# Kernel tuning notes

Measured on AMD Instinct MI355X. Metric: run time of the kernel, lower is better.

Reference implementation:

```python
import jax, jax.numpy as jnp
import numpy as np

B, T, D, H, STRIDE, MLP = 2, 2048, 1024, 16, 8, 4096
HD = D // H
EPS = 1e-5


def _ln(x, g, b):
    m = x.mean(-1, keepdims=True)
    v = x.var(-1, keepdims=True)
    return (x - m) * jax.lax.rsqrt(v + EPS) * g + b


def setup_inputs() -> dict:
    key = jax.random.key(0)
    ks = jax.random.split(key, 6)
    s = lambda k, shape: (jax.random.normal(k, shape, jnp.float32) * 0.02)
    return {
        "x": jax.random.normal(ks[0], (B, T, D), jnp.float32),
        "w_in": s(ks[1], (3 * D, D)),   # torch in_proj_weight
        "b_in": jnp.zeros((3 * D,), jnp.float32),
        "w_out": s(ks[2], (D, D)),      # attn out_proj
        "b_out": jnp.zeros((D,), jnp.float32),
        "w1": s(ks[3], (MLP, D)),       # mlp first Linear (torch layout [out,in])
        "b1": jnp.zeros((MLP,), jnp.float32),
        "w2": s(ks[4], (D, MLP)),       # mlp second Linear
        "b2": jnp.zeros((D,), jnp.float32),
        "ln1_g": jnp.ones((D,), jnp.float32),
        "ln1_b": jnp.zeros((D,), jnp.float32),
        "ln2_g": jnp.ones((D,), jnp.float32),
        "ln2_b": jnp.zeros((D,), jnp.float32),
    }


def reference(x, w_in, b_in, w_out, b_out, w1, b1, w2, b2,
              ln1_g, ln1_b, ln2_g, ln2_b):
    Bs, Ts, Ds = x.shape
    xn = _ln(x, ln1_g, ln1_b)
    # fused qkv projection (torch Linear: y = x @ W.T + b)
    qkv = xn @ w_in.T + b_in                              # [B,T,3D]
    q, k, v = jnp.split(qkv, 3, axis=-1)
    to_heads = lambda t: t.reshape(Bs, Ts, H, HD).transpose(0, 2, 1, 3)
    q, k, v = to_heads(q), to_heads(k), to_heads(v)       # [B,H,T,hd]
    scores = jnp.einsum("bhqd,bhkd->bhqk", q, k) / jnp.sqrt(jnp.float32(HD))
    # mask: rows at multiples of STRIDE attend everywhere; others only to self
    idx = jnp.arange(Ts)
    allowed = ((idx % STRIDE) == 0)[:, None] | (idx[:, None] == idx[None, :])
    scores = jnp.where(allowed, scores, -jnp.inf)
    attn = jax.nn.softmax(scores, axis=-1)
    o = jnp.einsum("bhqk,bhkd->bhqd", attn, v)            # [B,H,T,hd]
    o = o.transpose(0, 2, 1, 3).reshape(Bs, Ts, Ds)
    o = o @ w_out.T + b_out
    x = x + o
    xn = _ln(x, ln2_g, ln2_b)
    h = jax.nn.gelu(xn @ w1.T + b1, approximate=False)    # torch nn.GELU default = exact
    x = x + (h @ w2.T + b2)
    return x
```

## Files before the change

kernel.cpp:

```cpp
#include <hip/hip_runtime.h>

#define D_ 1024
#define T_ 2048
#define B_ 2
#define H_ 16
#define MLP_ 4096
#define NTOK (B_*T_)
#define QG 256
#define L2E 1.44269504088896340736f

typedef float f32x4 __attribute__((ext_vector_type(4)));
typedef __bf16 bf16x8 __attribute__((ext_vector_type(8)));

__device__ __forceinline__ unsigned short f2bf(float f) {
  unsigned int u = __float_as_uint(f);
  u += 0x7fff + ((u >> 16) & 1);
  return (unsigned short)(u >> 16);
}

__device__ __forceinline__ float wave_sum(float v) {
  for (int o = 32; o > 0; o >>= 1) v += __shfl_down(v, o, 64);
  return v;
}

__device__ __forceinline__ void gload16(const unsigned short* g, unsigned short* l) {
  __builtin_amdgcn_global_load_lds(
      (const __attribute__((address_space(1))) void*)g,
      (__attribute__((address_space(3))) void*)l, 16, 0, 0);
}

#define N4_WIN  786432
#define N4_WOUT 262144
#define N4_W1   1048576
#define N4_W2   1048576
__global__ void cast_all_kernel(const float* __restrict__ w_in,
                                const float* __restrict__ w_out,
                                const float* __restrict__ w1,
                                const float* __restrict__ w2,
                                unsigned short* __restrict__ o_in,
                                unsigned short* __restrict__ o_out,
                                unsigned short* __restrict__ o1,
                                unsigned short* __restrict__ o2) {
  int i = blockIdx.x * 256 + threadIdx.x;
  const float* src; unsigned short* dst; int j = i;
  if (i < N4_WIN) { src = w_in; dst = o_in; }
  else if ((j -= N4_WIN) < N4_WOUT) { src = w_out; dst = o_out; }
  else if ((j -= N4_WOUT) < N4_W1) { src = w1; dst = o1; }
  else { j -= N4_W1; src = w2; dst = o2; }
  float4 v = ((const float4*)src)[j];
  ushort4 o;
  o.x = f2bf(v.x); o.y = f2bf(v.y); o.z = f2bf(v.z); o.w = f2bf(v.w);
  ((ushort4*)dst)[j] = o;
}

__global__ void ln_kernel(const float* __restrict__ x, const float* __restrict__ g,
                          const float* __restrict__ b, unsigned short* __restrict__ out) {
  int row = blockIdx.x;
  int tid = threadIdx.x;
  int wave = tid >> 6, lane = tid & 63;
  float4 v = ((const float4*)(x + (size_t)row * D_))[tid];
  float s  = v.x + v.y + v.z + v.w;
  float s2 = v.x*v.x + v.y*v.y + v.z*v.z + v.w*v.w;
  s = wave_sum(s); s2 = wave_sum(s2);
  __shared__ float r1[4], r2[4];
  if (lane == 0) { r1[wave] = s; r2[wave] = s2; }
  __syncthreads();
  float ts  = r1[0] + r1[1] + r1[2] + r1[3];
  float ts2 = r2[0] + r2[1] + r2[2] + r2[3];
  float mean = ts * (1.0f / D_);
  float var  = ts2 * (1.0f / D_) - mean * mean;
  float rs = rsqrtf(var + 1e-5f);
  float4 gv = ((const float4*)g)[tid];
  float4 bv = ((const float4*)b)[tid];
  ushort4 o;
  o.x = f2bf((v.x - mean) * rs * gv.x + bv.x);
  o.y = f2bf((v.y - mean) * rs * gv.y + bv.y);
  o.z = f2bf((v.z - mean) * rs * gv.z + bv.z);
  o.w = f2bf((v.w - mean) * rs * gv.w + bv.w);
  ((ushort4*)(out + (size_t)row * D_))[tid] = o;
}

__global__ void reduce_ln_kernel(const float* __restrict__ part,
                                 const float* __restrict__ x,
                                 const float* __restrict__ bias,
                                 const float* __restrict__ g,
                                 const float* __restrict__ b,
                                 float* __restrict__ x1,
                                 unsigned short* __restrict__ xn2) {
  int row = blockIdx.x;
  int tid = threadIdx.x;
  int wave = tid >> 6, lane = tid & 63;
  size_t base = (size_t)row * (D_ / 4) + tid;
  float4 v = ((const float4*)x)[base];
  float4 bo = ((const float4*)bias)[tid];
  v.x += bo.x; v.y += bo.y; v.z += bo.z; v.w += bo.w;
#pragma unroll
  for (int c = 0; c < 2; ++c) {
    float4 p = ((const float4*)part)[(size_t)c * (NTOK * (D_ / 4)) + base];
    v.x += p.x; v.y += p.y; v.z += p.z; v.w += p.w;
  }
  ((float4*)x1)[base] = v;
  float s  = v.x + v.y + v.z + v.w;
  float s2 = v.x*v.x + v.y*v.y + v.z*v.z + v.w*v.w;
  s = wave_sum(s); s2 = wave_sum(s2);
  __shared__ float r1[4], r2[4];
  if (lane == 0) { r1[wave] = s; r2[wave] = s2; }
  __syncthreads();
  float ts  = r1[0] + r1[1] + r1[2] + r1[3];
  float ts2 = r2[0] + r2[1] + r2[2] + r2[3];
  float mean = ts * (1.0f / D_);
  float var  = ts2 * (1.0f / D_) - mean * mean;
  float rs = rsqrtf(var + 1e-5f);
  float4 gv = ((const float4*)g)[tid];
  float4 bv = ((const float4*)b)[tid];
  ushort4 o;
  o.x = f2bf((v.x - mean) * rs * gv.x + bv.x);
  o.y = f2bf((v.y - mean) * rs * gv.y + bv.y);
  o.z = f2bf((v.z - mean) * rs * gv.z + bv.z);
  o.w = f2bf((v.w - mean) * rs * gv.w + bv.w);
  ((ushort4*)xn2)[base] = o;
}

__global__ void reduce_out_kernel(const float* __restrict__ part,
                                  const float* __restrict__ x1,
                                  const float* __restrict__ bias,
                                  float* __restrict__ out) {
  int i = blockIdx.x * 256 + threadIdx.x;
  float4 v = ((const float4*)x1)[i];
  float4 bo = ((const float4*)bias)[i & (D_ / 4 - 1)];
  v.x += bo.x; v.y += bo.y; v.z += bo.z; v.w += bo.w;
#pragma unroll
  for (int c = 0; c < 4; ++c) {
    float4 p = ((const float4*)part)[(size_t)c * (NTOK * (D_ / 4)) + i];
    v.x += p.x; v.y += p.y; v.z += p.z; v.w += p.w;
  }
  ((float4*)out)[i] = v;
}

template<int EPI, int SWIZ, int LDA, int LDB, int LDC>
__global__ __launch_bounds__(256)
void gemm_kernel(const unsigned short* __restrict__ A, size_t sA,
                 const unsigned short* __restrict__ Bm, size_t sB,
                 void* __restrict__ Cv, size_t sC,
                 const float* __restrict__ bias,
                 unsigned short* __restrict__ aux1,
                 unsigned short* __restrict__ aux2,
                 int K, int nx, int ny, int kshift) {
  __shared__ __align__(16) unsigned short As[128 * 64];
  __shared__ __align__(16) unsigned short Bs[128 * 64];
  const int flat = blockIdx.x;
  int bx, by;
  if (SWIZ == 1) {
    bx = flat / ny; by = flat - bx * ny;
  } else {
    const int sxc = nx >> 1;
    const int nSuper = sxc * (ny >> 2);
    int s = flat % nSuper, pos = flat / nSuper;
    int sx = s % sxc, sy = s / sxc;
    bx = sx * 2 + (pos & 1);
    by = sy * 4 + (pos >> 1);
  }
  const int bz = blockIdx.z;
  const int batch = bz >> kshift;
  const int kOff  = (bz & ((1 << kshift) - 1)) * K;
  const int m0 = by * 128;
  const int n0 = bx * 128;
  const int tid = threadIdx.x;
  const int lane = tid & 63, wave = tid >> 6;
  const int wm = (wave >> 1) * 64, wn = (wave & 1) * 64;
  const int fr = lane & 15, q = lane >> 4;
  const int f0 = ((q)     ^ (fr & 7)) << 3;
  const int f1 = ((4 + q) ^ (fr & 7)) << 3;

  const unsigned short* aP[4];
  const unsigned short* bP[4];
  unsigned short* dA[4];
  unsigned short* dB[4];
#pragma unroll
  for (int p = 0; p < 4; ++p) {
    int l = p * 256 + tid;
    int r = l >> 3;
    int cg = (l & 7) ^ (r & 7);
    aP[p] = A  + (size_t)batch * sA + kOff + (size_t)(m0 + r) * LDA + cg * 8;
    bP[p] = Bm + (size_t)batch * sB + kOff + (size_t)(n0 + r) * LDB + cg * 8;
    dA[p] = &As[l * 8];
    dB[p] = &Bs[l * 8];
  }

  f32x4 acc[4][4] = {};
  for (int ko = 0; ko < K; ko += 64) {
    __syncthreads();
#pragma unroll
    for (int p = 0; p < 4; ++p) {
      gload16(aP[p], dA[p]); gload16(bP[p], dB[p]);
      aP[p] += 64; bP[p] += 64;
    }
    __syncthreads();
    {
      bf16x8 af[4], bfr[4];
#pragma unroll
      for (int i = 0; i < 4; ++i) af[i]  = *(const bf16x8*)&As[(wm + i * 16 + fr) * 64 + f0];
#pragma unroll
      for (int j = 0; j < 4; ++j) bfr[j] = *(const bf16x8*)&Bs[(wn + j * 16 + fr) * 64 + f0];
#pragma unroll
      for (int i = 0; i < 4; ++i)
#pragma unroll
        for (int j = 0; j < 4; ++j)
          acc[i][j] = __builtin_amdgcn_mfma_f32_16x16x32_bf16(af[i], bfr[j], acc[i][j], 0, 0, 0);
    }
    {
      bf16x8 af[4], bfr[4];
#pragma unroll
      for (int i = 0; i < 4; ++i) af[i]  = *(const bf16x8*)&As[(wm + i * 16 + fr) * 64 + f1];
#pragma unroll
      for (int j = 0; j < 4; ++j) bfr[j] = *(const bf16x8*)&Bs[(wn + j * 16 + fr) * 64 + f1];
#pragma unroll
      for (int i = 0; i < 4; ++i)
#pragma unroll
        for (int j = 0; j < 4; ++j)
          acc[i][j] = __builtin_amdgcn_mfma_f32_16x16x32_bf16(af[i], bfr[j], acc[i][j], 0, 0, 0);
    }
  }

  const int col = lane & 15, rbase = (lane >> 4) * 4;
#pragma unroll
  for (int i = 0; i < 4; ++i) {
#pragma unroll
    for (int j = 0; j < 4; ++j) {
      int gn = n0 + wn + j * 16 + col;
      int gmb = m0 + wm + i * 16 + rbase;
      float bv = (EPI == 2 || EPI == 8) ? bias[gn] : 0.0f;
#pragma unroll
      for (int r = 0; r < 4; ++r) {
        int gm = gmb + r;
        float v = acc[i][j][r] + bv;
        if (EPI == 2) {
          float u = v * (1.5957691216f + 0.0713548162f * v * v);
          float gl = v / (1.0f + exp2f(-L2E * u));
          ((unsigned short*)Cv)[(size_t)gm * LDC + gn] = f2bf(gl);
        } else if (EPI == 7) {
          ((float*)Cv)[(size_t)bz * sC + (size_t)gm * LDC + gn] = v;
        } else if (EPI == 8) {
          int sec = gn >> 10;
          int hh = (gn >> 6) & (H_ - 1);
          int dd = gn & 63;
          int t = gm & (T_ - 1);
          int b = gm >> 11;
          unsigned short bf = f2bf(v);
          if (sec == 0) {
            if (!(t & 7))
              aux1[(((size_t)(b * H_ + hh)) * QG + (t >> 3)) * 64 + dd] = bf;
          } else if (sec == 1) {
            aux2[(((size_t)(b * H_ + hh)) * T_ + t) * 64 + dd] = bf;
          } else {
            ((unsigned short*)Cv)[(size_t)gm * D_ + (gn - 2 * D_)] = bf;
          }
        }
      }
    }
  }
}

template<int EPI>
__global__ __launch_bounds__(512)
void gemm256_kernel(const unsigned short* __restrict__ A, int LDA,
                    const unsigned short* __restrict__ Bm, int LDB,
                    void* __restrict__ Cv, size_t sC, int LDC,
                    const float* __restrict__ bias, int K, int nxs) {
  __shared__ __align__(16) unsigned short As[2 * 16384];
  __shared__ __align__(16) unsigned short Bs[2 * 16384];
  const int tid = threadIdx.x;
  const int lane = tid & 63, w = tid >> 6;
  const int wm = w >> 2, wn = w & 3;
  const int fr = lane & 15, q = lane >> 4, xr = fr & 7;

  const int nwg = gridDim.x;
  const int bid = blockIdx.x;
  const int l = (bid & 7) * (nwg >> 3) + (bid >> 3);
  const int bx = l & ((1 << nxs) - 1), by = l >> nxs;
  const int m0 = by * 256, n0 = bx * 256;
  const int kOff = blockIdx.z * K;

  const unsigned short* aS[4];
  const unsigned short* bS[4];
#pragma unroll
  for (int s = 0; s < 4; ++s) {
    int ls = s * 512 + tid;
    int r = ls >> 3;
    int cg = (ls & 7) ^ (r & 7);
    aS[s] = A  + (size_t)(m0 + r) * LDA + kOff + cg * 8;
    bS[s] = Bm + (size_t)(n0 + r) * LDB + kOff + cg * 8;
  }
  const int NT = K >> 6;

#pragma unroll
  for (int s = 0; s < 4; ++s) {
    gload16(aS[s], &As[s * 4096 + tid * 8]);
    gload16(bS[s], &Bs[s * 4096 + tid * 8]);
  }
#pragma unroll
  for (int s = 0; s < 4; ++s) {
    gload16(aS[s] + 64, &As[16384 + s * 4096 + tid * 8]);
    gload16(bS[s] + 64, &Bs[16384 + s * 4096 + tid * 8]);
  }
  asm volatile("s_waitcnt vmcnt(8)");
  __builtin_amdgcn_sched_barrier(0);
  __builtin_amdgcn_s_barrier();
  __builtin_amdgcn_sched_barrier(0);

  const int aOff = ((wm * 128 + fr) << 7) + ((q ^ xr) << 4);
  const int bOff = ((wn * 64 + fr) << 7) + ((q ^ xr) << 4);

  f32x4 acc[8][4] = {};

  for (int t = 0; t < NT; ++t) {
    const int cb = (t & 1) << 15;
    const char* Ab = (const char*)As + cb;
    const char* Bb = (const char*)Bs + cb;
    unsigned short* Ad = (unsigned short*)((char*)As + cb);
    unsigned short* Bd = (unsigned short*)((char*)Bs + cb);
    const int ko2 = (t + 2) << 6;
    bf16x8 af[2][4], bfr[2][4];

#pragma unroll
    for (int i = 0; i < 4; ++i) {
      af[0][i] = *(const bf16x8*)(Ab + aOff + i * 2048);
      af[1][i] = *(const bf16x8*)(Ab + (aOff ^ 64) + i * 2048);
    }
#pragma unroll
    for (int j = 0; j < 2; ++j) {
      bfr[0][j] = *(const bf16x8*)(Bb + bOff + j * 2048);
      bfr[1][j] = *(const bf16x8*)(Bb + (bOff ^ 64) + j * 2048);
    }
    __builtin_amdgcn_sched_barrier(0);
    __builtin_amdgcn_s_barrier();
    __builtin_amdgcn_sched_barrier(0);
    __builtin_amdgcn_s_setprio(1);
#pragma unroll
    for (int i = 0; i < 4; ++i)
#pragma unroll
      for (int j = 0; j < 2; ++j) {
        acc[i][j] = __builtin_amdgcn_mfma_f32_16x16x32_bf16(af[0][i], bfr[0][j], acc[i][j], 0, 0, 0);
        acc[i][j] = __builtin_amdgcn_mfma_f32_16x16x32_bf16(af[1][i], bfr[1][j], acc[i][j], 0, 0, 0);
      }
    __builtin_amdgcn_s_setprio(0);
    __builtin_amdgcn_sched_barrier(0);
    __builtin_amdgcn_s_barrier();
    __builtin_amdgcn_sched_barrier(0);

#pragma unroll
    for (int j = 2; j < 4; ++j) {
      bfr[0][j] = *(const bf16x8*)(Bb + bOff + j * 2048);
      bfr[1][j] = *(const bf16x8*)(Bb + (bOff ^ 64) + j * 2048);
    }
    if (t + 2 < NT) {
      gload16(aS[0] + ko2, Ad + tid * 8);
      gload16(aS[2] + ko2, Ad + 2 * 4096 + tid * 8);
    }
    __builtin_amdgcn_sched_barrier(0);
    __builtin_amdgcn_s_barrier();
    __builtin_amdgcn_sched_barrier(0);
    __builtin_amdgcn_s_setprio(1);
#pragma unroll
    for (int i = 0; i < 4; ++i)
#pragma unroll
      for (int j = 0; j < 2; ++j) {
        acc[i][2 + j] = __builtin_amdgcn_mfma_f32_16x16x32_bf16(af[0][i], bfr[0][2 + j], acc[i][2 + j], 0, 0, 0);
        acc[i][2 + j] = __builtin_amdgcn_mfma_f32_16x16x32_bf16(af[1][i], bfr[1][2 + j], acc[i][2 + j], 0, 0, 0);
      }
    __builtin_amdgcn_s_setprio(0);
    __builtin_amdgcn_sched_barrier(0);
    __builtin_amdgcn_s_barrier();
    __builtin_amdgcn_sched_barrier(0);

#pragma unroll
    for (int i = 0; i < 4; ++i) {
      af[0][i] = *(const bf16x8*)(Ab + (aOff + 8192) + i * 2048);
      af[1][i] = *(const bf16x8*)(Ab + ((aOff + 8192) ^ 64) + i * 2048);
    }
    if (t + 2 < NT) {
      gload16(bS[0] + ko2, Bd + tid * 8);
      gload16(bS[1] + ko2, Bd + 4096 + tid * 8);
      gload16(bS[2] + ko2, Bd + 2 * 4096 + tid * 8);
      gload16(bS[3] + ko2, Bd + 3 * 4096 + tid * 8);
    }
    __builtin_amdgcn_sched_barrier(0);
    __builtin_amdgcn_s_barrier();
    __builtin_amdgcn_sched_barrier(0);
    __builtin_amdgcn_s_setprio(1);
#pragma unroll
    for (int i = 0; i < 4; ++i)
#pragma unroll
      for (int j = 0; j < 2; ++j) {
        acc[4 + i][j] = __builtin_amdgcn_mfma_f32_16x16x32_bf16(af[0][i], bfr[0][j], acc[4 + i][j], 0, 0, 0);
        acc[4 + i][j] = __builtin_amdgcn_mfma_f32_16x16x32_bf16(af[1][i], bfr[1][j], acc[4 + i][j], 0, 0, 0);
      }
    __builtin_amdgcn_s_setprio(0);
    __builtin_amdgcn_sched_barrier(0);
    __builtin_amdgcn_s_barrier();
    __builtin_amdgcn_sched_barrier(0);

    if (t + 2 < NT) {
      gload16(aS[1] + ko2, Ad + 4096 + tid * 8);
      gload16(aS[3] + ko2, Ad + 3 * 4096 + tid * 8);
    }
    if (t + 1 < NT) {
      if (t + 2 < NT) asm volatile("s_waitcnt vmcnt(8)");
      else            asm volatile("s_waitcnt vmcnt(0)");
    }
    __builtin_amdgcn_sched_barrier(0);
    __builtin_amdgcn_s_barrier();
    __builtin_amdgcn_sched_barrier(0);
    __builtin_amdgcn_s_setprio(1);
#pragma unroll
    for (int i = 0; i < 4; ++i)
#pragma unroll
      for (int j = 0; j < 2; ++j) {
        acc[4 + i][2 + j] = __builtin_amdgcn_mfma_f32_16x16x32_bf16(af[0][i], bfr[0][2 + j], acc[4 + i][2 + j], 0, 0, 0);
        acc[4 + i][2 + j] = __builtin_amdgcn_mfma_f32_16x16x32_bf16(af[1][i], bfr[1][2 + j], acc[4 + i][2 + j], 0, 0, 0);
      }
    __builtin_amdgcn_s_setprio(0);
    __builtin_amdgcn_sched_barrier(0);
    __builtin_amdgcn_s_barrier();
    __builtin_amdgcn_sched_barrier(0);
  }

  const int col = lane & 15, rbase = (lane >> 4) * 4;
  const int gm0 = m0 + wm * 128 + rbase;
  const int gn0 = n0 + wn * 64 + col;
#pragma unroll
  for (int mi = 0; mi < 8; ++mi) {
#pragma unroll
    for (int j = 0; j < 4; ++j) {
      int gn = gn0 + j * 16;
      float bv = (EPI == 2) ? bias[gn] : 0.0f;
#pragma unroll
      for (int r = 0; r < 4; ++r) {
        int gm = gm0 + mi * 16 + r;
        float v = acc[mi][j][r] + bv;
        if (EPI == 2) {
          float u = v * (1.5957691216f + 0.0713548162f * v * v);
          float gl = v / (1.0f + exp2f(-L2E * u));
          ((unsigned short*)Cv)[(size_t)gm * LDC + gn] = f2bf(gl);
        } else {
          ((float*)Cv)[(size_t)blockIdx.z * sC + (size_t)gm * LDC + gn] = v;
        }
      }
    }
  }
}

__global__ void vtrans_kernel(const unsigned short* __restrict__ vcomp,
                              unsigned short* __restrict__ Vt) {
  int blk = blockIdx.x;
  int tchunk = blk & 31;
  int bh = blk >> 5;
  int h = bh & (H_ - 1), b = bh >> 4;
  int t0 = tchunk * 64;
  __shared__ unsigned short ls[64][66];
  int tid = threadIdx.x;
#pragma unroll
  for (int it = 0; it < 16; ++it) {
    int linear = it * 256 + tid;
    int d = linear & 63, tl = linear >> 6;
    ls[d][tl] = vcomp[((size_t)(b * T_ + t0 + tl)) * D_ + h * 64 + d];
  }
  __syncthreads();
#pragma unroll
  for (int it = 0; it < 16; ++it) {
    int linear = it * 256 + tid;
    int tl = linear & 63, d = linear >> 6;
    Vt[((size_t)(bh * 64 + d)) * T_ + t0 + tl] = ls[d][tl];
  }
}

__global__ __launch_bounds__(256)
void flash_kernel(const unsigned short* __restrict__ Qg,
                  const unsigned short* __restrict__ Kh,
                  const unsigned short* __restrict__ Vt,
                  float* __restrict__ Opart,
                  float* __restrict__ ml) {
  const int kc = blockIdx.x, qt = blockIdx.y, bh = blockIdx.z;
  const int tid = threadIdx.x;
  const int lane = tid & 63, w = tid >> 6;
  const int fr = lane & 15, quad = lane >> 4;

  __shared__ __align__(16) unsigned short Qs[64 * 64];
  __shared__ __align__(16) unsigned short Ks[128 * 64];
  __shared__ __align__(16) unsigned short Vs[64 * 128];
  __shared__ __align__(16) unsigned short Ps[4 * 16 * 128];

  const unsigned short* Qbase = Qg + ((size_t)bh * 256 + qt * 64) * 64;
#pragma unroll
  for (int p = 0; p < 2; ++p) {
    int linear = p * 256 + tid;
    int r = linear >> 3, c = linear & 7;
    gload16(Qbase + r * 64 + (c ^ (r & 7)) * 8, &Qs[linear * 8]);
  }

  float m_run[4], l_run[4];
  f32x4 O[4] = {};
#pragma unroll
  for (int r = 0; r < 4; ++r) { m_run[r] = -3.0e38f; l_run[r] = 0.f; }

  const unsigned short* Kc = Kh + ((size_t)bh * T_ + kc * 512) * 64;
  const unsigned short* Vc = Vt + (size_t)bh * 64 * T_ + kc * 512;
  unsigned short* Pw = &Ps[w * 2048];
  const int arow = w * 16 + fr;

  for (int kt = 0; kt < 4; ++kt) {
    __syncthreads();
#pragma unroll
    for (int p = 0; p < 4; ++p) {
      int linear = p * 256 + tid;
      int r = linear >> 3, c = linear & 7;
      gload16(Kc + (size_t)(kt * 128 + r) * 64 + (c ^ (r & 7)) * 8, &Ks[linear * 8]);
    }
#pragma unroll
    for (int p = 0; p < 4; ++p) {
      int linear = p * 256 + tid;
      int r = linear >> 4, c = linear & 15;
      gload16(Vc + (size_t)r * T_ + kt * 128 + (c ^ (r & 7)) * 8, &Vs[linear * 8]);
    }
    __syncthreads();

    f32x4 s[8] = {};
    bf16x8 aq[2];
#pragma unroll
    for (int ks = 0; ks < 2; ++ks)
      aq[ks] = *(const bf16x8*)&Qs[arow * 64 + ((ks * 4 + quad) ^ (fr & 7)) * 8];
#pragma unroll
    for (int nf = 0; nf < 8; ++nf) {
      int krow = nf * 16 + fr;
#pragma unroll
      for (int ks = 0; ks < 2; ++ks) {
        bf16x8 bk = *(const bf16x8*)&Ks[krow * 64 + ((ks * 4 + quad) ^ (fr & 7)) * 8];
        s[nf] = __builtin_amdgcn_mfma_f32_16x16x32_bf16(aq[ks], bk, s[nf], 0, 0, 0);
      }
    }
    float alpha[4], rowsum[4];
#pragma unroll
    for (int r = 0; r < 4; ++r) {
      float mt = -3.0e38f;
#pragma unroll
      for (int nf = 0; nf < 8; ++nf) { s[nf][r] *= 0.125f; mt = fmaxf(mt, s[nf][r]); }
#pragma unroll
      for (int x = 1; x < 16; x <<= 1) mt = fmaxf(mt, __shfl_xor(mt, x, 64));
      float mn = fmaxf(m_run[r], mt);
      alpha[r] = exp2f((m_run[r] - mn) * L2E);
      m_run[r] = mn;
      rowsum[r] = 0.f;
    }
#pragma unroll
    for (int nf = 0; nf < 8; ++nf)
#pragma unroll
      for (int r = 0; r < 4; ++r) {
        float p = exp2f((s[nf][r] - m_run[r]) * L2E);
        s[nf][r] = p; rowsum[r] += p;
      }
#pragma unroll
    for (int r = 0; r < 4; ++r) {
#pragma unroll
      for (int x = 1; x < 16; x <<= 1) rowsum[r] += __shfl_xor(rowsum[r], x, 64);
      l_run[r] = l_run[r] * alpha[r] + rowsum[r];
    }
#pragma unroll
    for (int nf = 0; nf < 8; ++nf)
#pragma unroll
      for (int r = 0; r < 4; ++r) {
        int m = quad * 4 + r;
        int c = nf * 2 + (fr >> 3);
        Pw[m * 128 + ((c ^ (m & 7)) * 8) + (fr & 7)] = f2bf(s[nf][r]);
      }
#pragma unroll
    for (int nf2 = 0; nf2 < 4; ++nf2)
#pragma unroll
      for (int r = 0; r < 4; ++r) O[nf2][r] *= alpha[r];
#pragma unroll
    for (int ks2 = 0; ks2 < 4; ++ks2) {
      bf16x8 ap = *(const bf16x8*)&Pw[fr * 128 + (((ks2 * 4 + quad) ^ (fr & 7)) * 8)];
#pragma unroll
      for (int nf2 = 0; nf2 < 4; ++nf2) {
        int vrow = nf2 * 16 + fr;
        bf16x8 bv = *(const bf16x8*)&Vs[vrow * 128 + (((ks2 * 4 + quad) ^ (fr & 7)) * 8)];
        O[nf2] = __builtin_amdgcn_mfma_f32_16x16x32_bf16(ap, bv, O[nf2], 0, 0, 0);
      }
    }
  }

  int qbase = qt * 64 + w * 16;
  float* Ob = Opart + (((size_t)bh * 4 + kc) * 256 + qbase) * 64;
#pragma unroll
  for (int nf2 = 0; nf2 < 4; ++nf2)
#pragma unroll
    for (int r = 0; r < 4; ++r)
      Ob[(size_t)(quad * 4 + r) * 64 + nf2 * 16 + fr] = O[nf2][r];
  if (fr == 0) {
#pragma unroll
    for (int r = 0; r < 4; ++r) {
      size_t mi = ((((size_t)bh * 4 + kc) * 256) + qbase + quad * 4 + r) * 2;
      ml[mi] = m_run[r]; ml[mi + 1] = l_run[r];
    }
  }
}

__global__ void combine_kernel(const float* __restrict__ Opart,
                               const float* __restrict__ ml,
                               unsigned short* __restrict__ vcomp) {
  int idx = blockIdx.x * 256 + threadIdx.x;
  int c = idx & (D_ - 1);
  int qi = (idx >> 10) & (QG - 1);
  int b = idx >> 18;
  int h = c >> 6, d = c & 63;
  int bh = b * H_ + h;
  float m[4], l[4];
  float M = -3.0e38f;
#pragma unroll
  for (int ch = 0; ch < 4; ++ch) {
    size_t r = ((size_t)bh * 4 + ch) * 256 + qi;
    m[ch] = ml[r * 2]; l[ch] = ml[r * 2 + 1];
    M = fmaxf(M, m[ch]);
  }
  float osum = 0.f, lsum = 0.f;
#pragma unroll
  for (int ch = 0; ch < 4; ++ch) {
    size_t r = ((size_t)bh * 4 + ch) * 256 + qi;
    float wgt = exp2f((m[ch] - M) * L2E);
    osum += wgt * Opart[r * 64 + d];
    lsum += wgt * l[ch];
  }
  vcomp[((size_t)(b * T_ + qi * 8)) * D_ + c] = f2bf(osum / lsum);
}

extern "C" void kernel_launch(void* const* d_in, const int* in_sizes, int n_in,
                              void* d_out, int out_size, void* d_ws, size_t ws_size,
                              hipStream_t stream) {
  const float* x     = (const float*)d_in[0];
  const float* w_in  = (const float*)d_in[1];
  const float* b_in  = (const float*)d_in[2];
  const float* w_out = (const float*)d_in[3];
  const float* b_out = (const float*)d_in[4];
  const float* w1    = (const float*)d_in[5];
  const float* b1    = (const float*)d_in[6];
  const float* w2    = (const float*)d_in[7];
  const float* b2    = (const float*)d_in[8];
  const float* ln1_g = (const float*)d_in[9];
  const float* ln1_b = (const float*)d_in[10];
  const float* ln2_g = (const float*)d_in[11];
  const float* ln2_b = (const float*)d_in[12];
  float* out = (float*)d_out;

  char* ws = (char*)d_ws;
  size_t off = 0;
  auto alloc = [&](size_t bytes) -> void* {
    void* p = ws + off;
    off += (bytes + 255) & ~(size_t)255;
    return p;
  };
  unsigned short* w_inb = (unsigned short*)alloc((size_t)3 * D_ * D_ * 2);
  unsigned short* w_outb= (unsigned short*)alloc((size_t)D_ * D_ * 2);
  unsigned short* w1b   = (unsigned short*)alloc((size_t)MLP_ * D_ * 2);
  unsigned short* w2b   = (unsigned short*)alloc((size_t)D_ * MLP_ * 2);
  unsigned short* vcomp = (unsigned short*)alloc((size_t)NTOK * D_ * 2);
  float*          x1    = (float*)         alloc((size_t)NTOK * D_ * 4);
  unsigned short* xn2   = (unsigned short*)alloc((size_t)NTOK * D_ * 2);
  unsigned short* h     = (unsigned short*)alloc((size_t)NTOK * MLP_ * 2);
  char* U = (char*)alloc((size_t)4 * NTOK * D_ * 4);
  float*          P2    = (float*)U;
  unsigned short* xn    = (unsigned short*)U;
  unsigned short* Qg    = (unsigned short*)(U + 8388608);
  unsigned short* Kh    = (unsigned short*)(U + 12582912);
  unsigned short* Vt    = (unsigned short*)(U + 20971520);
  float*          Opart = (float*)         (U + 29360128);
  float*          mlbuf = (float*)         (U + 37748736);

  cast_all_kernel<<<(N4_WIN + N4_WOUT + N4_W1 + N4_W2) / 256, 256, 0, stream>>>(
      w_in, w_out, w1, w2, w_inb, w_outb, w1b, w2b);

  ln_kernel<<<NTOK, 256, 0, stream>>>(x, ln1_g, ln1_b, xn);

  gemm_kernel<8, 2, D_, D_, 3 * D_><<<dim3(24 * 32, 1, 1), 256, 0, stream>>>(
      xn, 0, w_inb, 0, vcomp, 0, b_in, Qg, Kh, D_, 24, 32, 0);

  vtrans_kernel<<<1024, 256, 0, stream>>>(vcomp, Vt);

  flash_kernel<<<dim3(4, 4, 32), 256, 0, stream>>>(Qg, Kh, Vt, Opart, mlbuf);

  combine_kernel<<<2048, 256, 0, stream>>>(Opart, mlbuf, vcomp);

  gemm_kernel<7, 1, D_, D_, D_><<<dim3(8 * 32, 1, 2), 256, 0, stream>>>(
      vcomp, 0, w_outb, 0, P2, (size_t)NTOK * D_, nullptr, nullptr, nullptr,
      512, 8, 32, 1);

  reduce_ln_kernel<<<NTOK, 256, 0, stream>>>(P2, x, b_out, ln2_g, ln2_b, x1, xn2);

  gemm256_kernel<2><<<dim3(256, 1, 1), 512, 0, stream>>>(
      xn2, D_, w1b, D_, h, 0, MLP_, b1, D_, 4);

  gemm256_kernel<7><<<dim3(64, 1, 4), 512, 0, stream>>>(
      h, MLP_, w2b, MLP_, P2, (size_t)NTOK * D_, D_, nullptr, 1024, 2);

  reduce_out_kernel<<<4096, 256, 0, stream>>>(P2, x1, b2, out);
}
```

Measured before the change: 332.5 us.

## Double-buffer 128-tile GEMM, use explicit M0 LDS loads, retile MLP down-projection

The 128x128 GEMM now double-buffers LDS with a two-stage prefetch driven by vmcnt waits, replacing the old load-sync-compute loop. It is used for the QKV, out-proj and MLP down-projection GEMMs. The down-projection moves from the 256-tile kernel with 4-way split-K to the 128-tile kernel with 2-way split-K, so the final reduction sums two partials instead of four. The 256-tile kernel issues global-to-LDS loads through inline asm that sets M0 once per wave, and many sched_barriers are removed. The aim is to hide global-load latency and cut split-K reduction traffic, at the cost of fewer waves per workgroup on the largest GEMM and more fragile inline-asm scheduling.

```diff
diff --git a/kernel.cpp b/kernel.cpp
--- a/kernel.cpp
+++ b/kernel.cpp
@@ -27,6 +27,17 @@
   __builtin_amdgcn_global_load_lds(
       (const __attribute__((address_space(1))) void*)g,
       (__attribute__((address_space(3))) void*)l, 16, 0, 0);
+}
+
+__device__ __forceinline__ unsigned ldsoff(const void* p) {
+  return (unsigned)(size_t)(const __attribute__((address_space(3))) void*)p;
+}
+
+__device__ __forceinline__ void agload16(const unsigned short* g, unsigned m0v) {
+  unsigned su = __builtin_amdgcn_readfirstlane(m0v);
+  asm volatile("s_mov_b32 m0, %0\n\t"
+               "global_load_lds_dwordx4 %1, off"
+               :: "s"(su), "v"(g) : "memory");
 }
 
 #define N4_WIN  786432
@@ -130,41 +141,33 @@
   float4 bo = ((const float4*)bias)[i & (D_ / 4 - 1)];
   v.x += bo.x; v.y += bo.y; v.z += bo.z; v.w += bo.w;
 #pragma unroll
-  for (int c = 0; c < 4; ++c) {
+  for (int c = 0; c < 2; ++c) {
     float4 p = ((const float4*)part)[(size_t)c * (NTOK * (D_ / 4)) + i];
     v.x += p.x; v.y += p.y; v.z += p.z; v.w += p.w;
   }
   ((float4*)out)[i] = v;
 }
 
-template<int EPI, int SWIZ, int LDA, int LDB, int LDC>
+template<int EPI>
 __global__ __launch_bounds__(256)
-void gemm_kernel(const unsigned short* __restrict__ A, size_t sA,
-                 const unsigned short* __restrict__ Bm, size_t sB,
-                 void* __restrict__ Cv, size_t sC,
-                 const float* __restrict__ bias,
-                 unsigned short* __restrict__ aux1,
-                 unsigned short* __restrict__ aux2,
-                 int K, int nx, int ny, int kshift) {
-  __shared__ __align__(16) unsigned short As[128 * 64];
-  __shared__ __align__(16) unsigned short Bs[128 * 64];
+void gemm128p_kernel(const unsigned short* __restrict__ A, int LDA,
+                     const unsigned short* __restrict__ Bm, int LDB,
+                     void* __restrict__ Cv, size_t sC, int LDC,
+                     const float* __restrict__ bias,
+                     unsigned short* __restrict__ aux1,
+                     unsigned short* __restrict__ aux2,
+                     int K, int nx, int ny) {
+  __shared__ __align__(16) unsigned short As[2 * 8192];
+  __shared__ __align__(16) unsigned short Bs[2 * 8192];
   const int flat = blockIdx.x;
-  int bx, by;
-  if (SWIZ == 1) {
-    bx = flat / ny; by = flat - bx * ny;
-  } else {
-    const int sxc = nx >> 1;
-    const int nSuper = sxc * (ny >> 2);
-    int s = flat % nSuper, pos = flat / nSuper;
-    int sx = s % sxc, sy = s / sxc;
-    bx = sx * 2 + (pos & 1);
-    by = sy * 4 + (pos >> 1);
-  }
-  const int bz = blockIdx.z;
-  const int batch = bz >> kshift;
-  const int kOff  = (bz & ((1 << kshift) - 1)) * K;
-  const int m0 = by * 128;
-  const int n0 = bx * 128;
+  const int sxc = nx >> 1;
+  const int nSuper = sxc * (ny >> 2);
+  int s = flat % nSuper, pos = flat / nSuper;
+  int sx = s % sxc, sy = s / sxc;
+  const int bx = sx * 2 + (pos & 1);
+  const int by = sy * 4 + (pos >> 1);
+  const int m0 = by * 128, n0 = bx * 128;
+  const int kOff = blockIdx.z * K;
   const int tid = threadIdx.x;
   const int lane = tid & 63, wave = tid >> 6;
   const int wm = (wave >> 1) * 64, wn = (wave & 1) * 64;
@@ -172,36 +175,46 @@
   const int f0 = ((q)     ^ (fr & 7)) << 3;
   const int f1 = ((4 + q) ^ (fr & 7)) << 3;
 
-  const unsigned short* aP[4];
-  const unsigned short* bP[4];
-  unsigned short* dA[4];
-  unsigned short* dB[4];
+  const unsigned short* aS[4];
+  const unsigned short* bS[4];
 #pragma unroll
   for (int p = 0; p < 4; ++p) {
     int l = p * 256 + tid;
     int r = l >> 3;
     int cg = (l & 7) ^ (r & 7);
-    aP[p] = A  + (size_t)batch * sA + kOff + (size_t)(m0 + r) * LDA + cg * 8;
-    bP[p] = Bm + (size_t)batch * sB + kOff + (size_t)(n0 + r) * LDB + cg * 8;
-    dA[p] = &As[l * 8];
-    dB[p] = &Bs[l * 8];
-  }
+    aS[p] = A  + (size_t)(m0 + r) * LDA + kOff + cg * 8;
+    bS[p] = Bm + (size_t)(n0 + r) * LDB + kOff + cg * 8;
+  }
+  const int NT = K >> 6;
+
+#pragma unroll
+  for (int p = 0; p < 4; ++p) {
+    gload16(aS[p], &As[p * 2048 + tid * 8]);
+    gload16(bS[p], &Bs[p * 2048 + tid * 8]);
+  }
+#pragma unroll
+  for (int p = 0; p < 4; ++p) {
+    gload16(aS[p] + 64, &As[8192 + p * 2048 + tid * 8]);
+    gload16(bS[p] + 64, &Bs[8192 + p * 2048 + tid * 8]);
+  }
+  asm volatile("s_waitcnt vmcnt(8)");
+  __builtin_amdgcn_sched_barrier(0);
+  __builtin_amdgcn_s_barrier();
 
   f32x4 acc[4][4] = {};
-  for (int ko = 0; ko < K; ko += 64) {
-    __syncthreads();
-#pragma unroll
-    for (int p = 0; p < 4; ++p) {
-      gload16(aP[p], dA[p]); gload16(bP[p], dB[p]);
-      aP[p] += 64; bP[p] += 64;
-    }
-    __syncthreads();
+  for (int t = 0; t < NT; ++t) {
+    const int cb = (t & 1) << 13;
+    const unsigned short* Ab = As + cb;
+    const unsigned short* Bb = Bs + cb;
+    unsigned short* Ad = As + cb;
+    unsigned short* Bd = Bs + cb;
+    const int ko2 = (t + 2) << 6;
     {
       bf16x8 af[4], bfr[4];
 #pragma unroll
-      for (int i = 0; i < 4; ++i) af[i]  = *(const bf16x8*)&As[(wm + i * 16 + fr) * 64 + f0];
-#pragma unroll
-      for (int j = 0; j < 4; ++j) bfr[j] = *(const bf16x8*)&Bs[(wn + j * 16 + fr) * 64 + f0];
+      for (int i = 0; i < 4; ++i) af[i]  = *(const bf16x8*)&Ab[(wm + i * 16 + fr) * 64 + f0];
+#pragma unroll
+      for (int j = 0; j < 4; ++j) bfr[j] = *(const bf16x8*)&Bb[(wn + j * 16 + fr) * 64 + f0];
 #pragma unroll
       for (int i = 0; i < 4; ++i)
 #pragma unroll
@@ -211,15 +224,29 @@
     {
       bf16x8 af[4], bfr[4];
 #pragma unroll
-      for (int i = 0; i < 4; ++i) af[i]  = *(const bf16x8*)&As[(wm + i * 16 + fr) * 64 + f1];
-#pragma unroll
-      for (int j = 0; j < 4; ++j) bfr[j] = *(const bf16x8*)&Bs[(wn + j * 16 + fr) * 64 + f1];
+      for (int i = 0; i < 4; ++i) af[i]  = *(const bf16x8*)&Ab[(wm + i * 16 + fr) * 64 + f1];
+#pragma unroll
+      for (int j = 0; j < 4; ++j) bfr[j] = *(const bf16x8*)&Bb[(wn + j * 16 + fr) * 64 + f1];
 #pragma unroll
       for (int i = 0; i < 4; ++i)
 #pragma unroll
         for (int j = 0; j < 4; ++j)
           acc[i][j] = __builtin_amdgcn_mfma_f32_16x16x32_bf16(af[i], bfr[j], acc[i][j], 0, 0, 0);
     }
+    __builtin_amdgcn_s_barrier();
+    if (t + 2 < NT) {
+#pragma unroll
+      for (int p = 0; p < 4; ++p) {
+        gload16(aS[p] + ko2, Ad + p * 2048 + tid * 8);
+        gload16(bS[p] + ko2, Bd + p * 2048 + tid * 8);
+      }
+    }
+    if (t + 1 < NT) {
+      if (t + 2 < NT) asm volatile("s_waitcnt vmcnt(8)");
+      else            asm volatile("s_waitcnt vmcnt(0)");
+      __builtin_amdgcn_sched_barrier(0);
+    }
+    __builtin_amdgcn_s_barrier();
   }
 
   const int col = lane & 15, rbase = (lane >> 4) * 4;
@@ -239,8 +266,8 @@
           float gl = v / (1.0f + exp2f(-L2E * u));
           ((unsigned short*)Cv)[(size_t)gm * LDC + gn] = f2bf(gl);
         } else if (EPI == 7) {
-          ((float*)Cv)[(size_t)bz * sC + (size_t)gm * LDC + gn] = v;
-        } else if (EPI == 8) {
+          ((float*)Cv)[(size_t)blockIdx.z * sC + (size_t)gm * LDC + gn] = v;
+        } else {
           int sec = gn >> 10;
           int hh = (gn >> 6) & (H_ - 1);
           int dd = gn & 63;
@@ -263,10 +290,11 @@
 
 template<int EPI>
 __global__ __launch_bounds__(512)
-void gemm256_kernel(const unsigned short* __restrict__ A, int LDA,
-                    const unsigned short* __restrict__ Bm, int LDB,
-                    void* __restrict__ Cv, size_t sC, int LDC,
-                    const float* __restrict__ bias, int K, int nxs) {
+void gemm256a_kernel(const unsigned short* __restrict__ A, int LDA,
+                     const unsigned short* __restrict__ Bm, int LDB,
+                     void* __restrict__ Cv, size_t sC, int LDC,
+                     const float* __restrict__ bias,
+                     int K, int nx) {
   __shared__ __align__(16) unsigned short As[2 * 16384];
   __shared__ __align__(16) unsigned short Bs[2 * 16384];
   const int tid = threadIdx.x;
@@ -277,7 +305,7 @@
   const int nwg = gridDim.x;
   const int bid = blockIdx.x;
   const int l = (bid & 7) * (nwg >> 3) + (bid >> 3);
-  const int bx = l & ((1 << nxs) - 1), by = l >> nxs;
+  const int bx = l % nx, by = l / nx;
   const int m0 = by * 256, n0 = bx * 256;
   const int kOff = blockIdx.z * K;
 
@@ -293,20 +321,22 @@
   }
   const int NT = K >> 6;
 
+  const unsigned asb = ldsoff(As), bsb = ldsoff(Bs);
+  const unsigned aW = asb + w * 1024, bW = bsb + w * 1024;
+
 #pragma unroll
   for (int s = 0; s < 4; ++s) {
-    gload16(aS[s], &As[s * 4096 + tid * 8]);
-    gload16(bS[s], &Bs[s * 4096 + tid * 8]);
+    agload16(aS[s], aW + s * 8192);
+    agload16(bS[s], bW + s * 8192);
   }
 #pragma unroll
   for (int s = 0; s < 4; ++s) {
-    gload16(aS[s] + 64, &As[16384 + s * 4096 + tid * 8]);
-    gload16(bS[s] + 64, &Bs[16384 + s * 4096 + tid * 8]);
+    agload16(aS[s] + 64, aW + 32768 + s * 8192);
+    agload16(bS[s] + 64, bW + 32768 + s * 8192);
   }
   asm volatile("s_waitcnt vmcnt(8)");
   __builtin_amdgcn_sched_barrier(0);
   __builtin_amdgcn_s_barrier();
-  __builtin_amdgcn_sched_barrier(0);
 
   const int aOff = ((wm * 128 + fr) << 7) + ((q ^ xr) << 4);
   const int bOff = ((wn * 64 + fr) << 7) + ((q ^ xr) << 4);
@@ -317,8 +347,7 @@
     const int cb = (t & 1) << 15;
     const char* Ab = (const char*)As + cb;
     const char* Bb = (const char*)Bs + cb;
-    unsigned short* Ad = (unsigned short*)((char*)As + cb);
-    unsigned short* Bd = (unsigned short*)((char*)Bs + cb);
+    const unsigned aWc = aW + cb, bWc = bW + cb;
     const int ko2 = (t + 2) << 6;
     bf16x8 af[2][4], bfr[2][4];
 
@@ -332,9 +361,7 @@
       bfr[0][j] = *(const bf16x8*)(Bb + bOff + j * 2048);
       bfr[1][j] = *(const bf16x8*)(Bb + (bOff ^ 64) + j * 2048);
     }
-    __builtin_amdgcn_sched_barrier(0);
-    __builtin_amdgcn_s_barrier();
-    __builtin_amdgcn_sched_barrier(0);
+    __builtin_amdgcn_s_barrier();
     __builtin_amdgcn_s_setprio(1);
 #pragma unroll
     for (int i = 0; i < 4; ++i)
@@ -344,9 +371,7 @@
         acc[i][j] = __builtin_amdgcn_mfma_f32_16x16x32_bf16(af[1][i], bfr[1][j], acc[i][j], 0, 0, 0);
       }
     __builtin_amdgcn_s_setprio(0);
-    __builtin_amdgcn_sched_barrier(0);
-    __builtin_amdgcn_s_barrier();
-    __builtin_amdgcn_sched_barrier(0);
+    __builtin_amdgcn_s_barrier();
 
 #pragma unroll
     for (int j = 2; j < 4; ++j) {
@@ -354,12 +379,10 @@
       bfr[1][j] = *(const bf16x8*)(Bb + (bOff ^ 64) + j * 2048);
     }
     if (t + 2 < NT) {
-      gload16(aS[0] + ko2, Ad + tid * 8);
-      gload16(aS[2] + ko2, Ad + 2 * 4096 + tid * 8);
-    }
-    __builtin_amdgcn_sched_barrier(0);
-    __builtin_amdgcn_s_barrier();
-    __builtin_amdgcn_sched_barrier(0);
+      agload16(aS[0] + ko2, aWc);
+      agload16(aS[2] + ko2, aWc + 16384);
+    }
+    __builtin_amdgcn_s_barrier();
     __builtin_amdgcn_s_setprio(1);
 #pragma unroll
     for (int i = 0; i < 4; ++i)
@@ -369,9 +392,7 @@
         acc[i][2 + j] = __builtin_amdgcn_mfma_f32_16x16x32_bf16(af[1][i], bfr[1][2 + j], acc[i][2 + j], 0, 0, 0);
       }
     __builtin_amdgcn_s_setprio(0);
-    __builtin_amdgcn_sched_barrier(0);
-    __builtin_amdgcn_s_barrier();
-    __builtin_amdgcn_sched_barrier(0);
+    __builtin_amdgcn_s_barrier();
 
 #pragma unroll
     for (int i = 0; i < 4; ++i) {
@@ -379,14 +400,12 @@
       af[1][i] = *(const bf16x8*)(Ab + ((aOff + 8192) ^ 64) + i * 2048);
     }
     if (t + 2 < NT) {
-      gload16(bS[0] + ko2, Bd + tid * 8);
-      gload16(bS[1] + ko2, Bd + 4096 + tid * 8);
-      gload16(bS[2] + ko2, Bd + 2 * 4096 + tid * 8);
-      gload16(bS[3] + ko2, Bd + 3 * 4096 + tid * 8);
-    }
-    __builtin_amdgcn_sched_barrier(0);
-    __builtin_amdgcn_s_barrier();
-    __builtin_amdgcn_sched_barrier(0);
+      agload16(bS[0] + ko2, bWc);
+      agload16(bS[1] + ko2, bWc + 8192);
+      agload16(bS[2] + ko2, bWc + 16384);
+      agload16(bS[3] + ko2, bWc + 24576);
+    }
+    __builtin_amdgcn_s_barrier();
     __builtin_amdgcn_s_setprio(1);
 #pragma unroll
     for (int i = 0; i < 4; ++i)
@@ -396,21 +415,18 @@
         acc[4 + i][j] = __builtin_amdgcn_mfma_f32_16x16x32_bf16(af[1][i], bfr[1][j], acc[4 + i][j], 0, 0, 0);
       }
     __builtin_amdgcn_s_setprio(0);
-    __builtin_amdgcn_sched_barrier(0);
-    __builtin_amdgcn_s_barrier();
-    __builtin_amdgcn_sched_barrier(0);
+    __builtin_amdgcn_s_barrier();
 
     if (t + 2 < NT) {
-      gload16(aS[1] + ko2, Ad + 4096 + tid * 8);
-      gload16(aS[3] + ko2, Ad + 3 * 4096 + tid * 8);
+      agload16(aS[1] + ko2, aWc + 8192);
+      agload16(aS[3] + ko2, aWc + 24576);
     }
     if (t + 1 < NT) {
       if (t + 2 < NT) asm volatile("s_waitcnt vmcnt(8)");
       else            asm volatile("s_waitcnt vmcnt(0)");
-    }
-    __builtin_amdgcn_sched_barrier(0);
-    __builtin_amdgcn_s_barrier();
-    __builtin_amdgcn_sched_barrier(0);
+      __builtin_amdgcn_sched_barrier(0);
+    }
+    __builtin_amdgcn_s_barrier();
     __builtin_amdgcn_s_setprio(1);
 #pragma unroll
     for (int i = 0; i < 4; ++i)
@@ -420,9 +436,7 @@
         acc[4 + i][2 + j] = __builtin_amdgcn_mfma_f32_16x16x32_bf16(af[1][i], bfr[1][2 + j], acc[4 + i][2 + j], 0, 0, 0);
       }
     __builtin_amdgcn_s_setprio(0);
-    __builtin_amdgcn_sched_barrier(0);
-    __builtin_amdgcn_s_barrier();
-    __builtin_amdgcn_sched_barrier(0);
+    __builtin_amdgcn_s_barrier();
   }
 
   const int col = lane & 15, rbase = (lane >> 4) * 4;
@@ -665,7 +679,7 @@
   float*          x1    = (float*)         alloc((size_t)NTOK * D_ * 4);
   unsigned short* xn2   = (unsigned short*)alloc((size_t)NTOK * D_ * 2);
   unsigned short* h     = (unsigned short*)alloc((size_t)NTOK * MLP_ * 2);
-  char* U = (char*)alloc((size_t)4 * NTOK * D_ * 4);
+  char* U = (char*)alloc((size_t)40 * 1024 * 1024);
   float*          P2    = (float*)U;
   unsigned short* xn    = (unsigned short*)U;
   unsigned short* Qg    = (unsigned short*)(U + 8388608);
@@ -679,8 +693,8 @@
 
   ln_kernel<<<NTOK, 256, 0, stream>>>(x, ln1_g, ln1_b, xn);
 
-  gemm_kernel<8, 2, D_, D_, 3 * D_><<<dim3(24 * 32, 1, 1), 256, 0, stream>>>(
-      xn, 0, w_inb, 0, vcomp, 0, b_in, Qg, Kh, D_, 24, 32, 0);
+  gemm128p_kernel<8><<<dim3(24 * 32, 1, 1), 256, 0, stream>>>(
+      xn, D_, w_inb, D_, vcomp, 0, 3 * D_, b_in, Qg, Kh, 1024, 24, 32);
 
   vtrans_kernel<<<1024, 256, 0, stream>>>(vcomp, Vt);
 
@@ -688,17 +702,18 @@
 
   combine_kernel<<<2048, 256, 0, stream>>>(Opart, mlbuf, vcomp);
 
-  gemm_kernel<7, 1, D_, D_, D_><<<dim3(8 * 32, 1, 2), 256, 0, stream>>>(
-      vcomp, 0, w_outb, 0, P2, (size_t)NTOK * D_, nullptr, nullptr, nullptr,
-      512, 8, 32, 1);
+  gemm128p_kernel<7><<<dim3(8 * 32, 1, 2), 256, 0, stream>>>(
+      vcomp, D_, w_outb, D_, P2, (size_t)NTOK * D_, D_, nullptr, nullptr, nullptr,
+      512, 8, 32);
 
   reduce_ln_kernel<<<NTOK, 256, 0, stream>>>(P2, x, b_out, ln2_g, ln2_b, x1, xn2);
 
-  gemm256_kernel<2><<<dim3(256, 1, 1), 512, 0, stream>>>(
-      xn2, D_, w1b, D_, h, 0, MLP_, b1, D_, 4);
-
-  gemm256_kernel<7><<<dim3(64, 1, 4), 512, 0, stream>>>(
-      h, MLP_, w2b, MLP_, P2, (size_t)NTOK * D_, D_, nullptr, 1024, 2);
+  gemm256a_kernel<2><<<dim3(256, 1, 1), 512, 0, stream>>>(
+      xn2, D_, w1b, D_, h, 0, MLP_, b1, 1024, 16);
+
+  gemm128p_kernel<7><<<dim3(8 * 32, 1, 2), 256, 0, stream>>>(
+      h, MLP_, w2b, MLP_, P2, (size_t)NTOK * D_, D_, nullptr, nullptr, nullptr,
+      2048, 8, 32);
 
   reduce_out_kernel<<<4096, 256, 0, stream>>>(P2, x1, b2, out);
 }
```

Result: no change. 327.4 us (-1.5%).
